# Optimization experiments

Measured on AMD Instinct MI355X. Metric: run time of the kernel, lower is better.

## Reference

```python
import jax, jax.numpy as jnp
import numpy as np

TOPK = 8  # n_activated_experts


def setup_inputs() -> dict:
    key = jax.random.key(0)
    k1, k2 = jax.random.split(key)
    tokens, dim, n_experts = 8192, 4096, 64
    x = jax.random.normal(k1, (tokens, dim), dtype=jnp.float32)
    weight = jax.random.normal(k2, (n_experts, dim), dtype=jnp.float32) * 0.02
    bias = jnp.zeros((n_experts,), dtype=jnp.float32)
    return {"x": x, "weight": weight, "bias": bias}


def reference(x, weight, bias):
    # scores: [tokens, n_experts]
    scores = jnp.einsum("td,ed->te", x, weight) + bias
    probs = jax.nn.softmax(scores, axis=-1)  # score_func == 'softmax'
    weights, indices = jax.lax.top_k(probs, TOPK)
    return probs, indices
```

## Files before the change

### kernel.cpp

```cpp
#include <hip/hip_runtime.h>
#include <math.h>

#define DIM     4096
#define NEXP    64
#define TOPK_N  8
#define TAU     2.0e-4f
#define TGB     64
#define KC      512
#define NKC     (DIM / KC)
#define NST     (KC / 32)

#define WS_WHI_OFF  0
#define WS_WLO_OFF  (512*1024)
#define WS_PART_OFF (1024*1024)

typedef __attribute__((ext_vector_type(8))) short short8;
typedef __attribute__((ext_vector_type(4))) float f32x4;

#define WALL __builtin_amdgcn_sched_barrier(0)

__device__ __forceinline__ void cvt8(float4 a0, float4 a1, short8& hv, short8& lv) {
    float f[8] = {a0.x, a0.y, a0.z, a0.w, a1.x, a1.y, a1.z, a1.w};
    union { short8 v; unsigned u[4]; } H, L;
    #pragma unroll
    for (int i = 0; i < 4; ++i) {
        unsigned b0 = __float_as_uint(f[2*i]);
        unsigned b1 = __float_as_uint(f[2*i+1]);
        float r0 = f[2*i]   - __uint_as_float(b0 & 0xffff0000u);
        float r1 = f[2*i+1] - __uint_as_float(b1 & 0xffff0000u);
        H.u[i] = (b0 >> 16) | (b1 & 0xffff0000u);
        L.u[i] = (__float_as_uint(r0) >> 16) | (__float_as_uint(r1) & 0xffff0000u);
    }
    hv = H.v; lv = L.v;
}

__device__ __forceinline__ void async16(void* lds, const void* g) {
    __builtin_amdgcn_global_load_lds(
        (const __attribute__((address_space(1))) unsigned int*)g,
        (__attribute__((address_space(3))) unsigned int*)lds, 16, 0, 0);
}

__global__ __launch_bounds__(256, 4)
void cvt_w_kernel(const float* __restrict__ w, unsigned short* __restrict__ whi,
                  unsigned short* __restrict__ wlo) {
    const int g = blockIdx.x * 256 + threadIdx.x;
    const float* p = w + (size_t)g * 8;
    union { short8 v; uint4 q; } H, L;
    float4 a0 = *(const float4*)(p);
    float4 a1 = *(const float4*)(p + 4);
    cvt8(a0, a1, H.v, L.v);
    *(uint4*)(whi + (size_t)g * 8) = H.q;
    *(uint4*)(wlo + (size_t)g * 8) = L.q;
}

__global__ __launch_bounds__(256, 4)
void zero_kernel(float* __restrict__ p) {
    const size_t g = (size_t)blockIdx.x * 256 + threadIdx.x;
    *(float4*)(p + g * 4) = (float4){0.f, 0.f, 0.f, 0.f};
}

template<int USE_PART>
__global__ __launch_bounds__(256, 4)
void gemm_part_kernel(const float* __restrict__ x, const unsigned short* __restrict__ whi,
                      const unsigned short* __restrict__ wlo, float* __restrict__ dst,
                      int ntok) {
    __shared__ float          A_lds[2][TGB][32];
    __shared__ unsigned short B_lds[2][NEXP][64];

    const int tid  = threadIdx.x;
    const int lane = tid & 63;
    const int wv   = tid >> 6;
    const int nl   = lane & 15;
    const int q    = lane >> 4;
    const int kc   = blockIdx.x & (NKC - 1);
    const int tg   = blockIdx.x >> 3;
    const int t0b  = tg * TGB;
    const int k0   = kc * KC;

    int arow[2], brow[2];
    const float* gA[2];
    const unsigned short* gB[2];
    #pragma unroll
    for (int i = 0; i < 2; ++i) {
        const int inst = wv * 2 + i;
        {
            const int r   = inst * 8 + (lane >> 3);
            const int scb = ((lane & 7) * 16) ^ ((r & 7) << 4);
            arow[i] = inst * 8;
            gA[i] = x + (size_t)(t0b + r) * DIM + k0 + (scb >> 2);
        }
        {
            const int e   = inst * 8 + (lane >> 3);
            const int scb = ((lane & 7) * 16) ^ ((e & 7) << 4);
            brow[i] = inst * 8;
            const unsigned short* base = (scb & 64) ? wlo : whi;
            gB[i] = base + (size_t)e * DIM + k0 + ((scb & 63) >> 1);
        }
    }

    f32x4 acc[4];
    #pragma unroll
    for (int nf = 0; nf < 4; ++nf) acc[nf] = (f32x4){0.f, 0.f, 0.f, 0.f};

#define STAGE(b_, st_) do {                                                    \
        async16(&A_lds[b_][arow[0]][0], gA[0] + (st_) * 32);                   \
        async16(&A_lds[b_][arow[1]][0], gA[1] + (st_) * 32);                   \
        async16(&B_lds[b_][brow[0]][0], gB[0] + (st_) * 32);                   \
        async16(&B_lds[b_][brow[1]][0], gB[1] + (st_) * 32);                   \
    } while (0)

#define COMPUTE(b_) do {                                                       \
        const char* Ab_ = (const char*)&A_lds[b_][wv * 16 + nl][0];            \
        const int swz_ = (nl & 7) << 4;                                        \
        float4 a0_ = *(const float4*)(Ab_ + ((q * 32) ^ swz_));                \
        float4 a1_ = *(const float4*)(Ab_ + ((q * 32 + 16) ^ swz_));           \
        short8 ahi_, alo_;                                                     \
        cvt8(a0_, a1_, ahi_, alo_);                                            \
        _Pragma("unroll")                                                      \
        for (int nf_ = 0; nf_ < 4; ++nf_) {                                    \
            const char* Bb_ = (const char*)&B_lds[b_][nf_ * 16 + nl][0];       \
            short8 bh_ = *(const short8*)(Bb_ + ((q * 16) ^ swz_));            \
            short8 bl_ = *(const short8*)(Bb_ + ((64 + q * 16) ^ swz_));       \
            acc[nf_] = __builtin_amdgcn_mfma_f32_16x16x32_bf16(ahi_, bl_, acc[nf_], 0, 0, 0); \
            acc[nf_] = __builtin_amdgcn_mfma_f32_16x16x32_bf16(alo_, bh_, acc[nf_], 0, 0, 0); \
            acc[nf_] = __builtin_amdgcn_mfma_f32_16x16x32_bf16(ahi_, bh_, acc[nf_], 0, 0, 0); \
        }                                                                      \
    } while (0)

    STAGE(0, 0);
    __syncthreads();
    #pragma unroll 2
    for (int st = 0; st < NST; ++st) {
        const int b = st & 1;
        if (st + 1 < NST) STAGE(b ^ 1, st + 1);
        WALL;
        COMPUTE(b);
        __syncthreads();
    }

#undef STAGE
#undef COMPUTE

    #pragma unroll
    for (int nf = 0; nf < 4; ++nf)
        #pragma unroll
        for (int r = 0; r < 4; ++r) {
            const int tok = t0b + wv * 16 + q * 4 + r;
            const int e   = nf * 16 + nl;
            if (USE_PART)
                dst[((size_t)tok * NKC + kc) * NEXP + e] = acc[nf][r];
            else
                atomicAdd(&dst[(size_t)tok * NEXP + e], acc[nf][r]);
        }
}

template<int USE_PART>
__global__ __launch_bounds__(256, 4)
void finish_kernel(const float* __restrict__ src, const float* __restrict__ bias,
                   const float* __restrict__ x, const float* __restrict__ wfp,
                   float* __restrict__ out, int ntok) {
    __shared__ float lds_s[4][68];
    __shared__ float t9[4][12];

    const int tid  = threadIdx.x;
    const int lane = tid & 63;
    const int wv   = tid >> 6;
    const int tok  = blockIdx.x * 4 + wv;

    float s;
    if (USE_PART) {
        const float* pr = src + (size_t)tok * NKC * NEXP;
        s = pr[lane];
        #pragma unroll
        for (int c = 1; c < NKC; ++c) s += pr[c * NEXP + lane];
    } else {
        s = src[(size_t)tok * NEXP + lane];
    }
    s += bias[lane];

    float m = s;
    #pragma unroll
    for (int off = 32; off > 0; off >>= 1)
        m = fmaxf(m, __shfl_xor(m, off, 64));
    const float ex = expf(s - m);
    float sum = ex;
    #pragma unroll
    for (int off = 32; off > 0; off >>= 1)
        sum += __shfl_xor(sum, off, 64);
    out[(size_t)tok * NEXP + lane] = ex / sum;

    lds_s[wv][lane] = s;
    int rank = 0;
    #pragma unroll
    for (int i = 0; i < 16; ++i) {
        const float4 v4 = *(const float4*)(&lds_s[wv][i * 4]);
        rank += (int)((v4.x > s) || (v4.x == s && (i * 4 + 0) < lane));
        rank += (int)((v4.y > s) || (v4.y == s && (i * 4 + 1) < lane));
        rank += (int)((v4.z > s) || (v4.z == s && (i * 4 + 2) < lane));
        rank += (int)((v4.w > s) || (v4.w == s && (i * 4 + 3) < lane));
    }
    float* __restrict__ out_idx = out + (size_t)ntok * NEXP;
    if (rank < TOPK_N + 1) t9[wv][rank] = s;
    if (rank < TOPK_N)
        out_idx[(size_t)tok * TOPK_N + rank] = (float)lane;

    float gap = 1e30f;
    if (lane < TOPK_N) gap = t9[wv][lane] - t9[wv][lane + 1];
    if (__any(gap < TAU)) {
        const float thr = t9[wv][TOPK_N] - TAU;
        const unsigned long long cmask = __ballot(s >= thr);
        double dscv = -1.0e300;
        unsigned long long mm = cmask;
        while (mm) {
            const int e = __builtin_ctzll(mm);
            mm &= mm - 1;
            const float* wr  = wfp + (size_t)e * DIM;
            const float* xrr = x + (size_t)tok * DIM;
            double a = 0.0;
            #pragma unroll 4
            for (int kk = 0; kk < 16; ++kk) {
                const int k = kk * 256 + lane * 4;
                const float4 wv4 = *(const float4*)(wr + k);
                const float4 xv  = *(const float4*)(xrr + k);
                a = fma((double)xv.x, (double)wv4.x, a);
                a = fma((double)xv.y, (double)wv4.y, a);
                a = fma((double)xv.z, (double)wv4.z, a);
                a = fma((double)xv.w, (double)wv4.w, a);
            }
            #pragma unroll
            for (int off = 32; off > 0; off >>= 1)
                a += __shfl_xor(a, off, 64);
            a += (double)bias[e];
            if (lane == e) dscv = a;
        }
        double cv = dscv;
        for (int r = 0; r < TOPK_N; ++r) {
            double bv = cv;
            int    bi = lane;
            #pragma unroll
            for (int off = 32; off > 0; off >>= 1) {
                const double ov = __shfl_xor(bv, off, 64);
                const int    oi = __shfl_xor(bi, off, 64);
                if (ov > bv || (ov == bv && oi < bi)) { bv = ov; bi = oi; }
            }
            if (lane == r)
                out_idx[(size_t)tok * TOPK_N + r] = (float)bi;
            if (lane == bi) cv = -1.0e301;
        }
    }
}

extern "C" void kernel_launch(void* const* d_in, const int* in_sizes, int n_in,
                              void* d_out, int out_size, void* d_ws, size_t ws_size,
                              hipStream_t stream) {
    const float* x  = (const float*)d_in[0];
    const float* w  = (const float*)d_in[1];
    const float* bs = (const float*)d_in[2];
    float* out = (float*)d_out;

    unsigned short* whi = (unsigned short*)((char*)d_ws + WS_WHI_OFF);
    unsigned short* wlo = (unsigned short*)((char*)d_ws + WS_WLO_OFF);

    const int ntok = in_sizes[0] / DIM;

    hipLaunchKernelGGL(cvt_w_kernel, dim3((NEXP * DIM) / 8 / 256), dim3(256), 0, stream,
                       w, whi, wlo);

    const size_t part_need = (size_t)WS_PART_OFF + (size_t)ntok * NKC * NEXP * sizeof(float);
    if (ws_size >= part_need) {
        float* part = (float*)((char*)d_ws + WS_PART_OFF);
        hipLaunchKernelGGL((gemm_part_kernel<1>), dim3((ntok / TGB) * NKC), dim3(256), 0, stream,
                           x, whi, wlo, part, ntok);
        hipLaunchKernelGGL((finish_kernel<1>), dim3(ntok / 4), dim3(256), 0, stream,
                           part, bs, x, w, out, ntok);
    } else {
        hipLaunchKernelGGL(zero_kernel, dim3((ntok * NEXP) / 1024), dim3(256), 0, stream, out);
        hipLaunchKernelGGL((gemm_part_kernel<0>), dim3((ntok / TGB) * NKC), dim3(256), 0, stream,
                           x, whi, wlo, out, ntok);
        hipLaunchKernelGGL((finish_kernel<0>), dim3(ntok / 4), dim3(256), 0, stream,
                           out, bs, x, w, out, ntok);
    }
}
```

Before: 228.4 us.

## Drop weight pre-conversion kernel and triple-buffer GEMM loads with vmcnt waits

Removes the separate kernel that split the fp32 weights into bf16 hi/lo arrays. The GEMM now loads fp32 weights straight into LDS and converts them inside the compute loop. The K loop moves from a double buffer to a triple buffer with two stages in flight. It waits with explicit s_waitcnt vmcnt plus a single barrier per iteration instead of two __syncthreads. This saves one launch and the staging traffic, but adds per-tile conversion ALU work and more LDS, and launch_bounds occupancy drops from 4 to 3.

```diff
diff --git a/kernel.cpp b/kernel.cpp
--- a/kernel.cpp
+++ b/kernel.cpp
@@ -10,10 +10,6 @@
 #define NKC     (DIM / KC)
 #define NST     (KC / 32)
 
-#define WS_WHI_OFF  0
-#define WS_WLO_OFF  (512*1024)
-#define WS_PART_OFF (1024*1024)
-
 typedef __attribute__((ext_vector_type(8))) short short8;
 typedef __attribute__((ext_vector_type(4))) float f32x4;
 
@@ -41,31 +37,17 @@
 }
 
 __global__ __launch_bounds__(256, 4)
-void cvt_w_kernel(const float* __restrict__ w, unsigned short* __restrict__ whi,
-                  unsigned short* __restrict__ wlo) {
-    const int g = blockIdx.x * 256 + threadIdx.x;
-    const float* p = w + (size_t)g * 8;
-    union { short8 v; uint4 q; } H, L;
-    float4 a0 = *(const float4*)(p);
-    float4 a1 = *(const float4*)(p + 4);
-    cvt8(a0, a1, H.v, L.v);
-    *(uint4*)(whi + (size_t)g * 8) = H.q;
-    *(uint4*)(wlo + (size_t)g * 8) = L.q;
-}
-
-__global__ __launch_bounds__(256, 4)
 void zero_kernel(float* __restrict__ p) {
     const size_t g = (size_t)blockIdx.x * 256 + threadIdx.x;
     *(float4*)(p + g * 4) = (float4){0.f, 0.f, 0.f, 0.f};
 }
 
 template<int USE_PART>
-__global__ __launch_bounds__(256, 4)
-void gemm_part_kernel(const float* __restrict__ x, const unsigned short* __restrict__ whi,
-                      const unsigned short* __restrict__ wlo, float* __restrict__ dst,
-                      int ntok) {
-    __shared__ float          A_lds[2][TGB][32];
-    __shared__ unsigned short B_lds[2][NEXP][64];
+__global__ __launch_bounds__(256, 3)
+void gemm_part_kernel(const float* __restrict__ x, const float* __restrict__ w,
+                      float* __restrict__ dst, int ntok) {
+    __shared__ float A_lds[3][TGB][32];
+    __shared__ float B_lds[3][NEXP][32];
 
     const int tid  = threadIdx.x;
     const int lane = tid & 63;
@@ -77,25 +59,17 @@
     const int t0b  = tg * TGB;
     const int k0   = kc * KC;
 
-    int arow[2], brow[2];
+    int arow[2];
     const float* gA[2];
-    const unsigned short* gB[2];
+    const float* gB[2];
     #pragma unroll
     for (int i = 0; i < 2; ++i) {
         const int inst = wv * 2 + i;
-        {
-            const int r   = inst * 8 + (lane >> 3);
-            const int scb = ((lane & 7) * 16) ^ ((r & 7) << 4);
-            arow[i] = inst * 8;
-            gA[i] = x + (size_t)(t0b + r) * DIM + k0 + (scb >> 2);
-        }
-        {
-            const int e   = inst * 8 + (lane >> 3);
-            const int scb = ((lane & 7) * 16) ^ ((e & 7) << 4);
-            brow[i] = inst * 8;
-            const unsigned short* base = (scb & 64) ? wlo : whi;
-            gB[i] = base + (size_t)e * DIM + k0 + ((scb & 63) >> 1);
-        }
+        const int r    = inst * 8 + (lane >> 3);
+        const int scb  = ((lane & 7) * 16) ^ ((r & 7) << 4);
+        arow[i] = inst * 8;
+        gA[i] = x + (size_t)(t0b + r) * DIM + k0 + (scb >> 2);
+        gB[i] = w + (size_t)r * DIM + k0 + (scb >> 2);
     }
 
     f32x4 acc[4];
@@ -105,13 +79,13 @@
 #define STAGE(b_, st_) do {                                                    \
         async16(&A_lds[b_][arow[0]][0], gA[0] + (st_) * 32);                   \
         async16(&A_lds[b_][arow[1]][0], gA[1] + (st_) * 32);                   \
-        async16(&B_lds[b_][brow[0]][0], gB[0] + (st_) * 32);                   \
-        async16(&B_lds[b_][brow[1]][0], gB[1] + (st_) * 32);                   \
+        async16(&B_lds[b_][arow[0]][0], gB[0] + (st_) * 32);                   \
+        async16(&B_lds[b_][arow[1]][0], gB[1] + (st_) * 32);                   \
     } while (0)
 
 #define COMPUTE(b_) do {                                                       \
+        const int swz_ = (nl & 7) << 4;                                        \
         const char* Ab_ = (const char*)&A_lds[b_][wv * 16 + nl][0];            \
-        const int swz_ = (nl & 7) << 4;                                        \
         float4 a0_ = *(const float4*)(Ab_ + ((q * 32) ^ swz_));                \
         float4 a1_ = *(const float4*)(Ab_ + ((q * 32 + 16) ^ swz_));           \
         short8 ahi_, alo_;                                                     \
@@ -119,8 +93,10 @@
         _Pragma("unroll")                                                      \
         for (int nf_ = 0; nf_ < 4; ++nf_) {                                    \
             const char* Bb_ = (const char*)&B_lds[b_][nf_ * 16 + nl][0];       \
-            short8 bh_ = *(const short8*)(Bb_ + ((q * 16) ^ swz_));            \
-            short8 bl_ = *(const short8*)(Bb_ + ((64 + q * 16) ^ swz_));       \
+            float4 b0_ = *(const float4*)(Bb_ + ((q * 32) ^ swz_));            \
+            float4 b1_ = *(const float4*)(Bb_ + ((q * 32 + 16) ^ swz_));       \
+            short8 bh_, bl_;                                                   \
+            cvt8(b0_, b1_, bh_, bl_);                                          \
             acc[nf_] = __builtin_amdgcn_mfma_f32_16x16x32_bf16(ahi_, bl_, acc[nf_], 0, 0, 0); \
             acc[nf_] = __builtin_amdgcn_mfma_f32_16x16x32_bf16(alo_, bh_, acc[nf_], 0, 0, 0); \
             acc[nf_] = __builtin_amdgcn_mfma_f32_16x16x32_bf16(ahi_, bh_, acc[nf_], 0, 0, 0); \
@@ -128,14 +104,19 @@
     } while (0)
 
     STAGE(0, 0);
-    __syncthreads();
-    #pragma unroll 2
+    STAGE(1, 1);
+    #pragma unroll 1
     for (int st = 0; st < NST; ++st) {
-        const int b = st & 1;
-        if (st + 1 < NST) STAGE(b ^ 1, st + 1);
+        if (st < NST - 1) {
+            asm volatile("s_waitcnt vmcnt(4)" ::: "memory");
+        } else {
+            asm volatile("s_waitcnt vmcnt(0)" ::: "memory");
+        }
+        __builtin_amdgcn_s_barrier();
+        __builtin_amdgcn_sched_barrier(0);
+        if (st + 2 < NST) STAGE((st + 2) % 3, st + 2);
         WALL;
-        COMPUTE(b);
-        __syncthreads();
+        COMPUTE(st % 3);
     }
 
 #undef STAGE
@@ -258,25 +239,19 @@
     const float* bs = (const float*)d_in[2];
     float* out = (float*)d_out;
 
-    unsigned short* whi = (unsigned short*)((char*)d_ws + WS_WHI_OFF);
-    unsigned short* wlo = (unsigned short*)((char*)d_ws + WS_WLO_OFF);
-
     const int ntok = in_sizes[0] / DIM;
 
-    hipLaunchKernelGGL(cvt_w_kernel, dim3((NEXP * DIM) / 8 / 256), dim3(256), 0, stream,
-                       w, whi, wlo);
-
-    const size_t part_need = (size_t)WS_PART_OFF + (size_t)ntok * NKC * NEXP * sizeof(float);
+    const size_t part_need = (size_t)ntok * NKC * NEXP * sizeof(float);
     if (ws_size >= part_need) {
-        float* part = (float*)((char*)d_ws + WS_PART_OFF);
+        float* part = (float*)d_ws;
         hipLaunchKernelGGL((gemm_part_kernel<1>), dim3((ntok / TGB) * NKC), dim3(256), 0, stream,
-                           x, whi, wlo, part, ntok);
+                           x, w, part, ntok);
         hipLaunchKernelGGL((finish_kernel<1>), dim3(ntok / 4), dim3(256), 0, stream,
                            part, bs, x, w, out, ntok);
     } else {
         hipLaunchKernelGGL(zero_kernel, dim3((ntok * NEXP) / 1024), dim3(256), 0, stream, out);
         hipLaunchKernelGGL((gemm_part_kernel<0>), dim3((ntok / TGB) * NKC), dim3(256), 0, stream,
-                           x, whi, wlo, out, ntok);
+                           x, w, out, ntok);
         hipLaunchKernelGGL((finish_kernel<0>), dim3(ntok / 4), dim3(256), 0, stream,
                            out, bs, x, w, out, ntok);
     }
```

Result: slower. 233.9 us (+2.4%).
